# Performance work log

Measured on AMD Instinct MI355X. Metric: run time of the kernel, lower is better.

Reference implementation:

```python
import jax, jax.numpy as jnp
import numpy as np

B, L, D = 8, 4096, 768
EPS = 1e-5


def layer_norm(x, g, b):
    mu = jnp.mean(x, axis=-1, keepdims=True)
    var = jnp.mean(jnp.square(x - mu), axis=-1, keepdims=True)
    return (x - mu) * jax.lax.rsqrt(var + EPS) * g + b


def conv1d_same(x_blc, w_oik, b_o):
    # x_blc: [B, L, C] -> torch Conv1d(C, C, 3, padding=1) on [B, C, L]
    x_ncw = jnp.swapaxes(x_blc, 1, 2)
    y = jax.lax.conv_general_dilated(
        x_ncw, w_oik, window_strides=(1,), padding=[(1, 1)],
        dimension_numbers=("NCW", "OIW", "NCW"))
    y = y + b_o[None, :, None]
    return jnp.swapaxes(y, 1, 2)


def simple_ssm(u, a_p, b_p, c_p, d_p):
    # Diagonal SSM: h_t = sigmoid(a)*h_{t-1} + b*u_t ; y_t = c*h_t + d*u_t
    a = jax.nn.sigmoid(a_p)  # [D]

    def step(h, ut):  # h, ut: [B, D]
        h = a * h + b_p * ut
        return h, c_p * h

    h0 = jnp.zeros((u.shape[0], u.shape[2]), u.dtype)
    _, y = jax.lax.scan(step, h0, jnp.swapaxes(u, 0, 1))  # y: [L, B, D]
    return jnp.swapaxes(y, 0, 1) + d_p * u


def setup_inputs() -> dict:
    key = jax.random.key(0)
    ks = jax.random.split(key, 16)
    s_lin = 1.0 / np.sqrt(D)
    s_conv = 1.0 / np.sqrt(3 * D)
    return {
        "x": jax.random.normal(ks[0], (B, L, D), jnp.float32),
        "ln_g": jnp.ones((D,), jnp.float32),
        "ln_b": jnp.zeros((D,), jnp.float32),
        "Wi": jax.random.normal(ks[1], (D, 2 * D), jnp.float32) * s_lin,
        "bi": jnp.zeros((2 * D,), jnp.float32),
        "Wf_conv": jax.random.normal(ks[2], (D, D, 3), jnp.float32) * s_conv,
        "bf_conv": jnp.zeros((D,), jnp.float32),
        "af": jax.random.normal(ks[3], (D,), jnp.float32),
        "bf": jax.random.normal(ks[4], (D,), jnp.float32) * 0.5,
        "cf": jax.random.normal(ks[5], (D,), jnp.float32) * 0.5,
        "df": jax.random.normal(ks[6], (D,), jnp.float32) * 0.5,
        "Wb_conv": jax.random.normal(ks[7], (D, D, 3), jnp.float32) * s_conv,
        "bb_conv": jnp.zeros((D,), jnp.float32),
        "ab": jax.random.normal(ks[8], (D,), jnp.float32),
        "bb": jax.random.normal(ks[9], (D,), jnp.float32) * 0.5,
        "cb": jax.random.normal(ks[10], (D,), jnp.float32) * 0.5,
        "db": jax.random.normal(ks[11], (D,), jnp.float32) * 0.5,
        "Wo": jax.random.normal(ks[12], (D, D), jnp.float32) * s_lin,
        "bo": jnp.zeros((D,), jnp.float32),
    }


def reference(x, ln_g, ln_b, Wi, bi, Wf_conv, bf_conv, af, bf, cf, df,
              Wb_conv, bb_conv, ab, bb, cb, db, Wo, bo):
    residual = x
    xn = layer_norm(x, ln_g, ln_b)
    proj = xn @ Wi + bi                      # [B, L, 2D]
    xg, z = proj[..., :D], proj[..., D:]
    # forward branch
    f = conv1d_same(xg, Wf_conv, bf_conv)
    f = simple_ssm(f, af, bf, cf, df)
    # backward branch (flip along sequence)
    b_in = jnp.flip(xg, axis=1)
    bb_out = conv1d_same(b_in, Wb_conv, bb_conv)
    bb_out = simple_ssm(bb_out, ab, bb, cb, db)
    bb_out = jnp.flip(bb_out, axis=1)
    zg = jax.nn.silu(z)
    y = f * zg + bb_out * zg
    return y @ Wo + bo + residual
```

## Files before the change

kernel.cpp:

```cpp
#include <hip/hip_runtime.h>
#include <cstdint>
#include <cstddef>
#include <math.h>

#define L_SEQ 4096
#define D_DIM 768
#define B_SZ 8
#define M_ROWS (B_SZ * L_SEQ)
#define CHUNK 64

typedef __bf16 bf16x8 __attribute__((ext_vector_type(8)));
typedef float floatx4 __attribute__((ext_vector_type(4)));

#define GLP(p)  ((__attribute__((address_space(1))) const void*)(const void*)(p))
#define LDSP(p) ((__attribute__((address_space(3))) void*)(void*)(p))

__global__ __launch_bounds__(256) void ln_kernel(const float* __restrict__ x,
                                                 const float* __restrict__ g,
                                                 const float* __restrict__ b,
                                                 __bf16* __restrict__ xn) {
  __shared__ float red[256];
  const int tid = threadIdx.x;
  const size_t row = blockIdx.x;
  const float* xr = x + row * D_DIM;
  float v0 = xr[tid];
  float v1 = xr[tid + 256];
  float v2 = xr[tid + 512];
  red[tid] = v0 + v1 + v2;
  __syncthreads();
  for (int off = 128; off > 0; off >>= 1) {
    if (tid < off) red[tid] += red[tid + off];
    __syncthreads();
  }
  float mu = red[0] * (1.0f / D_DIM);
  __syncthreads();
  float d0 = v0 - mu, d1 = v1 - mu, d2 = v2 - mu;
  red[tid] = d0 * d0 + d1 * d1 + d2 * d2;
  __syncthreads();
  for (int off = 128; off > 0; off >>= 1) {
    if (tid < off) red[tid] += red[tid + off];
    __syncthreads();
  }
  float rs = rsqrtf(red[0] * (1.0f / D_DIM) + 1e-5f);
  __bf16* xo = xn + row * D_DIM;
  xo[tid]       = (__bf16)(d0 * rs * g[tid]       + b[tid]);
  xo[tid + 256] = (__bf16)(d1 * rs * g[tid + 256] + b[tid + 256]);
  xo[tid + 512] = (__bf16)(d2 * rs * g[tid + 512] + b[tid + 512]);
}


#define VMW(n) asm volatile("s_waitcnt vmcnt(" #n ")" ::: "memory")
#define BARR   asm volatile("s_barrier" ::: "memory")
#define MF(a, b, c) __builtin_amdgcn_mfma_f32_16x16x32_bf16((a), (b), (c), 0, 0, 0)
#define LDV(off) (*(const bf16x8*)(smem + (off)))

#define RDA(BUF, MOFF) do { \
  aR0k0 = LDV((BUF)*65536 + aoff + (MOFF) + ck0);        aR0k1 = LDV((BUF)*65536 + aoff + (MOFF) + ck1); \
  aR1k0 = LDV((BUF)*65536 + aoff + (MOFF) + 2048 + ck0); aR1k1 = LDV((BUF)*65536 + aoff + (MOFF) + 2048 + ck1); \
  aR2k0 = LDV((BUF)*65536 + aoff + (MOFF) + 4096 + ck0); aR2k1 = LDV((BUF)*65536 + aoff + (MOFF) + 4096 + ck1); \
  aR3k0 = LDV((BUF)*65536 + aoff + (MOFF) + 6144 + ck0); aR3k1 = LDV((BUF)*65536 + aoff + (MOFF) + 6144 + ck1); \
} while (0)

#define RDB01(BUF) do { \
  bN0k0 = LDV((BUF)*65536 + boff + ck0);        bN0k1 = LDV((BUF)*65536 + boff + ck1); \
  bN1k0 = LDV((BUF)*65536 + boff + 2048 + ck0); bN1k1 = LDV((BUF)*65536 + boff + 2048 + ck1); \
} while (0)

#define RDB23(BUF) do { \
  bN2k0 = LDV((BUF)*65536 + boff + 4096 + ck0); bN2k1 = LDV((BUF)*65536 + boff + 4096 + ck1); \
  bN3k0 = LDV((BUF)*65536 + boff + 6144 + ck0); bN3k1 = LDV((BUF)*65536 + boff + 6144 + ck1); \
} while (0)

#define MMQ01(AI) do { \
  acc[(AI)+0][0] = MF(aR0k0, bN0k0, acc[(AI)+0][0]); acc[(AI)+0][0] = MF(aR0k1, bN0k1, acc[(AI)+0][0]); \
  acc[(AI)+0][1] = MF(aR0k0, bN1k0, acc[(AI)+0][1]); acc[(AI)+0][1] = MF(aR0k1, bN1k1, acc[(AI)+0][1]); \
  acc[(AI)+1][0] = MF(aR1k0, bN0k0, acc[(AI)+1][0]); acc[(AI)+1][0] = MF(aR1k1, bN0k1, acc[(AI)+1][0]); \
  acc[(AI)+1][1] = MF(aR1k0, bN1k0, acc[(AI)+1][1]); acc[(AI)+1][1] = MF(aR1k1, bN1k1, acc[(AI)+1][1]); \
  acc[(AI)+2][0] = MF(aR2k0, bN0k0, acc[(AI)+2][0]); acc[(AI)+2][0] = MF(aR2k1, bN0k1, acc[(AI)+2][0]); \
  acc[(AI)+2][1] = MF(aR2k0, bN1k0, acc[(AI)+2][1]); acc[(AI)+2][1] = MF(aR2k1, bN1k1, acc[(AI)+2][1]); \
  acc[(AI)+3][0] = MF(aR3k0, bN0k0, acc[(AI)+3][0]); acc[(AI)+3][0] = MF(aR3k1, bN0k1, acc[(AI)+3][0]); \
  acc[(AI)+3][1] = MF(aR3k0, bN1k0, acc[(AI)+3][1]); acc[(AI)+3][1] = MF(aR3k1, bN1k1, acc[(AI)+3][1]); \
} while (0)

#define MMQ23(AI) do { \
  acc[(AI)+0][2] = MF(aR0k0, bN2k0, acc[(AI)+0][2]); acc[(AI)+0][2] = MF(aR0k1, bN2k1, acc[(AI)+0][2]); \
  acc[(AI)+0][3] = MF(aR0k0, bN3k0, acc[(AI)+0][3]); acc[(AI)+0][3] = MF(aR0k1, bN3k1, acc[(AI)+0][3]); \
  acc[(AI)+1][2] = MF(aR1k0, bN2k0, acc[(AI)+1][2]); acc[(AI)+1][2] = MF(aR1k1, bN2k1, acc[(AI)+1][2]); \
  acc[(AI)+1][3] = MF(aR1k0, bN3k0, acc[(AI)+1][3]); acc[(AI)+1][3] = MF(aR1k1, bN3k1, acc[(AI)+1][3]); \
  acc[(AI)+2][2] = MF(aR2k0, bN2k0, acc[(AI)+2][2]); acc[(AI)+2][2] = MF(aR2k1, bN2k1, acc[(AI)+2][2]); \
  acc[(AI)+2][3] = MF(aR2k0, bN3k0, acc[(AI)+2][3]); acc[(AI)+2][3] = MF(aR2k1, bN3k1, acc[(AI)+2][3]); \
  acc[(AI)+3][2] = MF(aR3k0, bN2k0, acc[(AI)+3][2]); acc[(AI)+3][2] = MF(aR3k1, bN2k1, acc[(AI)+3][2]); \
  acc[(AI)+3][3] = MF(aR3k0, bN3k0, acc[(AI)+3][3]); acc[(AI)+3][3] = MF(aR3k1, bN3k1, acc[(AI)+3][3]); \
} while (0)

#define STAGE_A_HP(h, p, tkt, BUF) do { \
  const __bf16* _s; \
  if (MODE == 1) { \
    const int _kb = ((tkt) * 43) >> 9;                        \
    const int _io = (((tkt) - _kb * 12) << 6) + (_kb - 1) * D_DIM; \
    _s = ((unsigned)(lv##h##p + _kb - 1) < (unsigned)L_SEQ) ? (rb##h##p + _io) : zbuf; \
  } else { \
    _s = rb##h##p + (tkt) * 64; \
  } \
  __builtin_amdgcn_global_load_lds(GLP(_s), \
      LDSP(smem + (BUF)*65536 + (h)*8192 + (p)*16384 + dstw), 16, 0, 0); \
} while (0)

#define STAGE_B_HP(h, p, tkt, BUF) \
  __builtin_amdgcn_global_load_lds(GLP(pB##h##p + (tkt) * 64), \
      LDSP(smem + (BUF)*65536 + 32768 + (h)*16384 + (p)*8192 + dstw), 16, 0, 0)

#define TILE(T, BUF, VA, VC, SA1, SREST) do { \
   \
  VMW(VA); BARR; \
  RDB01(BUF); RDA(BUF, 0); \
  if (SA1) { STAGE_A_HP(1, 0, (T) + 1, (BUF) ^ 1); STAGE_A_HP(1, 1, (T) + 1, (BUF) ^ 1); } \
  __builtin_amdgcn_s_setprio(1); MMQ01(0); __builtin_amdgcn_s_setprio(0); \
   \
  BARR; \
  RDB23(BUF); \
  if (SREST) { STAGE_A_HP(0, 0, (T) + 2, (BUF)); STAGE_A_HP(0, 1, (T) + 2, (BUF)); } \
  __builtin_amdgcn_s_setprio(1); MMQ23(0); __builtin_amdgcn_s_setprio(0); \
   \
  VMW(VC); BARR; \
  RDA(BUF, 8192); \
  if (SREST) { STAGE_B_HP(0, 0, (T) + 2, (BUF)); STAGE_B_HP(0, 1, (T) + 2, (BUF)); } \
  __builtin_amdgcn_s_setprio(1); MMQ01(4); __builtin_amdgcn_s_setprio(0); \
   \
  if (SREST) { STAGE_B_HP(1, 0, (T) + 2, (BUF)); STAGE_B_HP(1, 1, (T) + 2, (BUF)); } \
  __builtin_amdgcn_s_setprio(1); MMQ23(4); __builtin_amdgcn_s_setprio(0); \
} while (0)

template<int MODE, int NT, int NN>
__global__ __launch_bounds__(512) void gemm256_kernel(
    const __bf16* __restrict__ A, const __bf16* __restrict__ Bt,
    const float* __restrict__ bias_lo, const float* __restrict__ bias_hi,
    const float* __restrict__ resid,
    __bf16* __restrict__ out0, __bf16* __restrict__ out1,
    float* __restrict__ outf, const __bf16* __restrict__ zbuf) {
  extern __shared__ char smem[];
  constexpr int K = NT * 64;
  constexpr int nwg = NN * (M_ROWS / 256);
  constexpr int cpx = nwg / 8;
  const int bid = blockIdx.x;
  const int wgs = (bid & 7) * cpx + (bid >> 3);
  const int tileN = wgs % NN;
  const int tileM = wgs / NN;
  const int tid  = (int)threadIdx.x;
  const int w    = tid >> 6;
  const int lane = tid & 63;
  const int l15  = lane & 15;
  const int quad = lane >> 4;
  const int wm   = w >> 2;
  const int wn   = w & 3;

  const int srow = tid >> 3;
  const int ce   = ((tid & 7) ^ (srow & 7)) << 3;
  const int dstw = w << 10;

  const int aoff = (wm * 128 + l15) * 128;
  const int boff = 32768 + (wn * 64 + l15) * 128;
  const int ck0  = (quad ^ (l15 & 7)) << 4;
  const int ck1  = ((4 | quad) ^ (l15 & 7)) << 4;

  const __bf16* pB00 = Bt + (size_t)(tileN * 256 + srow) * K + ce;
  const __bf16* pB01 = Bt + (size_t)(tileN * 256 + 64 + srow) * K + ce;
  const __bf16* pB10 = Bt + (size_t)(tileN * 256 + 128 + srow) * K + ce;
  const __bf16* pB11 = Bt + (size_t)(tileN * 256 + 192 + srow) * K + ce;

  const __bf16 *rb00, *rb01, *rb10, *rb11;
  int lv00 = 0, lv01 = 0, lv10 = 0, lv11 = 0;
  {
    const int g00 = tileM * 256 + srow;
    const int g01 = tileM * 256 + 128 + srow;
    const int g10 = tileM * 256 + 64 + srow;
    const int g11 = tileM * 256 + 192 + srow;
    if (MODE == 1) {
      rb00 = A + (size_t)g00 * D_DIM + ce; lv00 = g00 & (L_SEQ - 1);
      rb01 = A + (size_t)g01 * D_DIM + ce; lv01 = g01 & (L_SEQ - 1);
      rb10 = A + (size_t)g10 * D_DIM + ce; lv10 = g10 & (L_SEQ - 1);
      rb11 = A + (size_t)g11 * D_DIM + ce; lv11 = g11 & (L_SEQ - 1);
    } else {
      rb00 = A + (size_t)g00 * K + ce;
      rb01 = A + (size_t)g01 * K + ce;
      rb10 = A + (size_t)g10 * K + ce;
      rb11 = A + (size_t)g11 * K + ce;
    }
  }

  bf16x8 aR0k0, aR0k1, aR1k0, aR1k1, aR2k0, aR2k1, aR3k0, aR3k1;
  bf16x8 bN0k0, bN0k1, bN1k0, bN1k1, bN2k0, bN2k1, bN3k0, bN3k1;
  floatx4 acc[8][4];
#pragma unroll
  for (int i = 0; i < 8; ++i)
#pragma unroll
    for (int j = 0; j < 4; ++j)
#pragma unroll
      for (int r = 0; r < 4; ++r) acc[i][j][r] = 0.0f;

  STAGE_A_HP(0, 0, 0, 0); STAGE_A_HP(0, 1, 0, 0);
  STAGE_B_HP(0, 0, 0, 0); STAGE_B_HP(0, 1, 0, 0);
  STAGE_B_HP(1, 0, 0, 0); STAGE_B_HP(1, 1, 0, 0);
  STAGE_A_HP(1, 0, 0, 0); STAGE_A_HP(1, 1, 0, 0);
  STAGE_A_HP(0, 0, 1, 1); STAGE_A_HP(0, 1, 1, 1);
  STAGE_B_HP(0, 0, 1, 1); STAGE_B_HP(0, 1, 1, 1);
  STAGE_B_HP(1, 0, 1, 1); STAGE_B_HP(1, 1, 1, 1);

  for (int it = 0; it < (NT - 2) / 2; ++it) {
    const int T0 = it * 2;
    TILE(T0,     0, 8, 10, 1, 1);
    TILE(T0 + 1, 1, 8, 10, 1, 1);
  }
  TILE(NT - 2, 0, 8, 8, 1, 0);
  TILE(NT - 1, 1, 2, 0, 0, 0);

  const int rowb = tileM * 256 + wm * 128 + quad * 4;
  const int colb = tileN * 256 + wn * 64 + l15;
#pragma unroll
  for (int mi = 0; mi < 8; ++mi) {
#pragma unroll
    for (int nj = 0; nj < 4; ++nj) {
      const int col = colb + nj * 16;
      float bv;
      if (MODE == 3) bv = bias_lo[col];
      else bv = (col < D_DIM) ? bias_lo[col] : bias_hi[col - D_DIM];
#pragma unroll
      for (int r = 0; r < 4; ++r) {
        const int row = rowb + mi * 16 + r;
        float v = acc[mi][nj][r] + bv;
        if (MODE == 3) {
          const size_t o = (size_t)row * D_DIM + col;
          outf[o] = v + resid[o];
        } else if (MODE == 0) {
          if (col < D_DIM) out0[(size_t)row * D_DIM + col] = (__bf16)v;
          else out1[(size_t)row * D_DIM + (col - D_DIM)] = (__bf16)(v / (1.0f + expf(-v)));
        } else {
          if (col < D_DIM) out0[(size_t)row * D_DIM + col] = (__bf16)v;
          else out1[(size_t)row * D_DIM + (col - D_DIM)] = (__bf16)v;
        }
      }
    }
  }
}

__global__ __launch_bounds__(256) void scan1_kernel(
    const float* __restrict__ ap0, const float* __restrict__ bp0,
    const float* __restrict__ ap1, const float* __restrict__ bp1,
    const __bf16* __restrict__ u0, const __bf16* __restrict__ u1,
    float* __restrict__ hl) {
  int idx = blockIdx.x * 256 + threadIdx.x;
  int dg = idx % 96;
  int rest = idx / 96;
  int chunk = rest & 63;
  int tb = rest >> 6;
  int tensor = tb >> 3;
  int b = tb & 7;
  const float* ap = (tensor ? ap1 : ap0) + dg * 8;
  const float* bp = (tensor ? bp1 : bp0) + dg * 8;
  const __bf16* u = (tensor ? u1 : u0) +
      ((size_t)(b * L_SEQ + chunk * CHUNK + (tensor ? CHUNK - 1 : 0))) * D_DIM + dg * 8;
  const int st = tensor ? -D_DIM : D_DIM;
  float a[8], bb[8], h[8];
#pragma unroll
  for (int j = 0; j < 8; ++j) {
    a[j] = 1.0f / (1.0f + expf(-ap[j]));
    bb[j] = bp[j];
    h[j] = 0.0f;
  }
  for (int t = 0; t < CHUNK; ++t) {
    bf16x8 uv = *(const bf16x8*)u;
#pragma unroll
    for (int j = 0; j < 8; ++j) h[j] = a[j] * h[j] + bb[j] * (float)uv[j];
    u += st;
  }
  float* o = hl + (size_t)(tb * 64 + chunk) * D_DIM + dg * 8;
#pragma unroll
  for (int j = 0; j < 8; ++j) o[j] = h[j];
}

__global__ __launch_bounds__(256) void scan2_kernel(
    const float* __restrict__ ap0, const float* __restrict__ ap1,
    float* __restrict__ hl) {
  int idx = blockIdx.x * 256 + threadIdx.x;
  int d = idx % D_DIM;
  int tb = idx / D_DIM;
  int tensor = tb >> 3;
  const float* ap = tensor ? ap1 : ap0;
  float a = 1.0f / (1.0f + expf(-ap[d]));
  float aT = a * a;  aT *= aT;  aT *= aT;  aT *= aT;  aT *= aT;  aT *= aT;
  float* p = hl + (size_t)tb * 64 * D_DIM + d + (tensor ? 63 * D_DIM : 0);
  const int st = tensor ? -D_DIM : D_DIM;
  float carry = 0.0f;
  for (int c = 0; c < 64; ++c) {
    float tmp = *p;
    *p = carry;
    carry = aT * carry + tmp;
    p += st;
  }
}

__global__ __launch_bounds__(256) void scan3_kernel(
    const float* __restrict__ ap0, const float* __restrict__ bp0,
    const float* __restrict__ cp0, const float* __restrict__ dp0,
    const float* __restrict__ ap1, const float* __restrict__ bp1,
    const float* __restrict__ cp1, const float* __restrict__ dp1,
    __bf16* __restrict__ u0, __bf16* __restrict__ u1,
    const float* __restrict__ hl) {
  int idx = blockIdx.x * 256 + threadIdx.x;
  int dg = idx % 96;
  int rest = idx / 96;
  int chunk = rest & 63;
  int tb = rest >> 6;
  int tensor = tb >> 3;
  int b = tb & 7;
  const float* ap = (tensor ? ap1 : ap0) + dg * 8;
  const float* bp = (tensor ? bp1 : bp0) + dg * 8;
  const float* cp = (tensor ? cp1 : cp0) + dg * 8;
  const float* dp = (tensor ? dp1 : dp0) + dg * 8;
  __bf16* u = (tensor ? u1 : u0) +
      ((size_t)(b * L_SEQ + chunk * CHUNK + (tensor ? CHUNK - 1 : 0))) * D_DIM + dg * 8;
  const int st = tensor ? -D_DIM : D_DIM;
  const float* hp = hl + (size_t)(tb * 64 + chunk) * D_DIM + dg * 8;
  float a[8], bb[8], cc[8], dd[8], h[8];
#pragma unroll
  for (int j = 0; j < 8; ++j) {
    a[j] = 1.0f / (1.0f + expf(-ap[j]));
    bb[j] = bp[j]; cc[j] = cp[j]; dd[j] = dp[j];
    h[j] = hp[j];
  }
  for (int t = 0; t < CHUNK; ++t) {
    bf16x8 uv = *(const bf16x8*)u;
    bf16x8 ov;
#pragma unroll
    for (int j = 0; j < 8; ++j) {
      float xv = (float)uv[j];
      h[j] = a[j] * h[j] + bb[j] * xv;
      ov[j] = (__bf16)(cc[j] * h[j] + dd[j] * xv);
    }
    *(bf16x8*)u = ov;
    u += st;
  }
}

__global__ __launch_bounds__(256) void gate_kernel(const __bf16* __restrict__ f,
                                                   const __bf16* __restrict__ bbuf,
                                                   const __bf16* __restrict__ zg,
                                                   __bf16* __restrict__ y) {
  size_t e = ((size_t)blockIdx.x * 256 + threadIdx.x) * 8;
  bf16x8 f8 = *(const bf16x8*)(f + e);
  bf16x8 b8 = *(const bf16x8*)(bbuf + e);
  bf16x8 z8 = *(const bf16x8*)(zg + e);
  bf16x8 o;
#pragma unroll
  for (int j = 0; j < 8; ++j)
    o[j] = (__bf16)(((float)f8[j] + (float)b8[j]) * (float)z8[j]);
  *(bf16x8*)(y + e) = o;
}

__global__ __launch_bounds__(256) void tr_kernel(const float* __restrict__ in,
                                                 __bf16* __restrict__ out,
                                                 int Kdim, int Ndim) {
  int idx = blockIdx.x * 256 + threadIdx.x;
  if (idx >= Kdim * Ndim) return;
  int n = idx / Kdim;
  int k = idx - n * Kdim;
  out[idx] = (__bf16)in[(size_t)k * Ndim + n];
}

__global__ __launch_bounds__(256) void trconv_kernel(const float* __restrict__ in,
                                                     __bf16* __restrict__ out,
                                                     int rev) {
  int idx = blockIdx.x * 256 + threadIdx.x;
  if (idx >= D_DIM * 2304) return;
  int o = idx / 2304;
  int rem = idx - o * 2304;
  int k = rem / D_DIM;
  int i = rem - k * D_DIM;
  int ks = rev ? (2 - k) : k;
  out[idx] = (__bf16)in[(size_t)o * 2304 + i * 3 + ks];
}

__global__ void zero_kernel(__bf16* z) { z[threadIdx.x] = (__bf16)0.0f; }

extern "C" void kernel_launch(void* const* d_in, const int* in_sizes, int n_in,
                              void* d_out, int out_size, void* d_ws, size_t ws_size,
                              hipStream_t stream) {
  const float* x    = (const float*)d_in[0];
  const float* ln_g = (const float*)d_in[1];
  const float* ln_b = (const float*)d_in[2];
  const float* Wi   = (const float*)d_in[3];
  const float* bi   = (const float*)d_in[4];
  const float* Wf   = (const float*)d_in[5];
  const float* bfc  = (const float*)d_in[6];
  const float* af   = (const float*)d_in[7];
  const float* bfp  = (const float*)d_in[8];
  const float* cfp  = (const float*)d_in[9];
  const float* dfp  = (const float*)d_in[10];
  const float* Wb   = (const float*)d_in[11];
  const float* bbc  = (const float*)d_in[12];
  const float* ab   = (const float*)d_in[13];
  const float* bbp  = (const float*)d_in[14];
  const float* cbp  = (const float*)d_in[15];
  const float* dbp  = (const float*)d_in[16];
  const float* Wo   = (const float*)d_in[17];
  const float* bo   = (const float*)d_in[18];
  float* out = (float*)d_out;

  char* ws = (char*)d_ws;
  const size_t BLD = (size_t)B_SZ * L_SEQ * D_DIM;
  __bf16* ws0 = (__bf16*)(ws);
  __bf16* ws1 = (__bf16*)(ws + BLD * 2);
  __bf16* ws2 = (__bf16*)(ws + BLD * 4);
  __bf16* ws3 = (__bf16*)(ws + BLD * 6);
  __bf16* wit  = (__bf16*)(ws + BLD * 8);
  __bf16* wcat = wit + (size_t)1536 * 768;
  __bf16* wot  = wcat + (size_t)1536 * 2304;
  __bf16* zbuf = wot + (size_t)768 * 768;
  float* hl = (float*)(ws + BLD * 2);
  const size_t needed = BLD * 8 +
      ((size_t)1536 * 768 + (size_t)1536 * 2304 + (size_t)768 * 768) * 2 + 256;
  if (ws_size < needed) return;

  static bool attr_done = false;
  if (!attr_done) {
    (void)hipFuncSetAttribute(reinterpret_cast<const void*>(&gemm256_kernel<0, 12, 6>),
                              hipFuncAttributeMaxDynamicSharedMemorySize, 131072);
    (void)hipFuncSetAttribute(reinterpret_cast<const void*>(&gemm256_kernel<1, 36, 6>),
                              hipFuncAttributeMaxDynamicSharedMemorySize, 131072);
    (void)hipFuncSetAttribute(reinterpret_cast<const void*>(&gemm256_kernel<3, 12, 3>),
                              hipFuncAttributeMaxDynamicSharedMemorySize, 131072);
    attr_done = true;
  }

  zero_kernel<<<1, 128, 0, stream>>>(zbuf);
  tr_kernel<<<(768 * 1536 + 255) / 256, 256, 0, stream>>>(Wi, wit, 768, 1536);
  trconv_kernel<<<(768 * 2304 + 255) / 256, 256, 0, stream>>>(Wf, wcat, 0);
  trconv_kernel<<<(768 * 2304 + 255) / 256, 256, 0, stream>>>(Wb, wcat + (size_t)768 * 2304, 1);
  tr_kernel<<<(768 * 768 + 255) / 256, 256, 0, stream>>>(Wo, wot, 768, 768);

  ln_kernel<<<M_ROWS, 256, 0, stream>>>(x, ln_g, ln_b, ws0);

  gemm256_kernel<0, 12, 6><<<768, 512, 131072, stream>>>(
      ws0, wit, bi, bi + 768, nullptr, ws1, ws2, nullptr, zbuf);

  gemm256_kernel<1, 36, 6><<<768, 512, 131072, stream>>>(
      ws1, wcat, bfc, bbc, nullptr, ws0, ws3, nullptr, zbuf);

  scan1_kernel<<<384, 256, 0, stream>>>(af, bfp, ab, bbp, ws0, ws3, hl);
  scan2_kernel<<<48, 256, 0, stream>>>(af, ab, hl);
  scan3_kernel<<<384, 256, 0, stream>>>(af, bfp, cfp, dfp, ab, bbp, cbp, dbp, ws0, ws3, hl);

  gate_kernel<<<12288, 256, 0, stream>>>(ws0, ws3, ws2, ws1);

  gemm256_kernel<3, 12, 3><<<384, 512, 131072, stream>>>(
      ws1, wot, bo, bo, x, nullptr, nullptr, out, zbuf);
}
```

Before: 746.4 us.

## Fuse SSM output pass with gating into one kernel

The final SSM scan pass and the elementwise gate kernel are merged. Each thread first runs the forward-branch scan in place, then runs the backward-branch scan and combines it directly with the forward result and the SiLU gate, writing the gated output. This drops the backward-branch output write and the separate gate kernel's reads, and removes one launch. To make room, the chunk-carry buffer moves into the now-unused conv weight area, since the gate output buffer it used to share is written during the same kernel. In exchange the grid is halved to 192 blocks, each thread doing two sequential 64-step chains, which lowers parallelism and latency hiding.

New measurement: 773.5 us. +3.6%, slower.

```diff
diff --git a/kernel.cpp b/kernel.cpp
--- a/kernel.cpp
+++ b/kernel.cpp
@@ -299,62 +299,83 @@
   }
 }
 
-__global__ __launch_bounds__(256) void scan3_kernel(
+__global__ __launch_bounds__(256) void ssm_gate_kernel(
     const float* __restrict__ ap0, const float* __restrict__ bp0,
     const float* __restrict__ cp0, const float* __restrict__ dp0,
     const float* __restrict__ ap1, const float* __restrict__ bp1,
     const float* __restrict__ cp1, const float* __restrict__ dp1,
-    __bf16* __restrict__ u0, __bf16* __restrict__ u1,
+    __bf16* __restrict__ u0, const __bf16* __restrict__ u1,
+    const __bf16* __restrict__ zg, __bf16* __restrict__ y,
     const float* __restrict__ hl) {
   int idx = blockIdx.x * 256 + threadIdx.x;
   int dg = idx % 96;
   int rest = idx / 96;
   int chunk = rest & 63;
-  int tb = rest >> 6;
-  int tensor = tb >> 3;
-  int b = tb & 7;
-  const float* ap = (tensor ? ap1 : ap0) + dg * 8;
-  const float* bp = (tensor ? bp1 : bp0) + dg * 8;
-  const float* cp = (tensor ? cp1 : cp0) + dg * 8;
-  const float* dp = (tensor ? dp1 : dp0) + dg * 8;
-  __bf16* u = (tensor ? u1 : u0) +
-      ((size_t)(b * L_SEQ + chunk * CHUNK + (tensor ? CHUNK - 1 : 0))) * D_DIM + dg * 8;
-  const int st = tensor ? -D_DIM : D_DIM;
-  const float* hp = hl + (size_t)(tb * 64 + chunk) * D_DIM + dg * 8;
-  float a[8], bb[8], cc[8], dd[8], h[8];
-#pragma unroll
-  for (int j = 0; j < 8; ++j) {
-    a[j] = 1.0f / (1.0f + expf(-ap[j]));
-    bb[j] = bp[j]; cc[j] = cp[j]; dd[j] = dp[j];
-    h[j] = hp[j];
-  }
-  for (int t = 0; t < CHUNK; ++t) {
-    bf16x8 uv = *(const bf16x8*)u;
-    bf16x8 ov;
+  int b = rest >> 6;
+  const size_t rowbase = (size_t)(b * L_SEQ + chunk * CHUNK) * D_DIM + dg * 8;
+
+  {
+    const float* ap = ap0 + dg * 8;
+    const float* bp = bp0 + dg * 8;
+    const float* cp = cp0 + dg * 8;
+    const float* dp = dp0 + dg * 8;
+    const float* hp = hl + (size_t)(b * 64 + chunk) * D_DIM + dg * 8;
+    float a[8], bb[8], cc[8], dd[8], h[8];
 #pragma unroll
     for (int j = 0; j < 8; ++j) {
-      float xv = (float)uv[j];
-      h[j] = a[j] * h[j] + bb[j] * xv;
-      ov[j] = (__bf16)(cc[j] * h[j] + dd[j] * xv);
-    }
-    *(bf16x8*)u = ov;
-    u += st;
-  }
-}
-
-__global__ __launch_bounds__(256) void gate_kernel(const __bf16* __restrict__ f,
-                                                   const __bf16* __restrict__ bbuf,
-                                                   const __bf16* __restrict__ zg,
-                                                   __bf16* __restrict__ y) {
-  size_t e = ((size_t)blockIdx.x * 256 + threadIdx.x) * 8;
-  bf16x8 f8 = *(const bf16x8*)(f + e);
-  bf16x8 b8 = *(const bf16x8*)(bbuf + e);
-  bf16x8 z8 = *(const bf16x8*)(zg + e);
-  bf16x8 o;
-#pragma unroll
-  for (int j = 0; j < 8; ++j)
-    o[j] = (__bf16)(((float)f8[j] + (float)b8[j]) * (float)z8[j]);
-  *(bf16x8*)(y + e) = o;
+      a[j] = 1.0f / (1.0f + expf(-ap[j]));
+      bb[j] = bp[j]; cc[j] = cp[j]; dd[j] = dp[j];
+      h[j] = hp[j];
+    }
+    __bf16* p = u0 + rowbase;
+    for (int t = 0; t < CHUNK; ++t) {
+      bf16x8 uv = *(const bf16x8*)p;
+      bf16x8 ov;
+#pragma unroll
+      for (int j = 0; j < 8; ++j) {
+        float xv = (float)uv[j];
+        h[j] = a[j] * h[j] + bb[j] * xv;
+        ov[j] = (__bf16)(cc[j] * h[j] + dd[j] * xv);
+      }
+      *(bf16x8*)p = ov;
+      p += D_DIM;
+    }
+  }
+
+  {
+    const float* ap = ap1 + dg * 8;
+    const float* bp = bp1 + dg * 8;
+    const float* cp = cp1 + dg * 8;
+    const float* dp = dp1 + dg * 8;
+    const float* hp = hl + (size_t)((8 + b) * 64 + chunk) * D_DIM + dg * 8;
+    float a[8], bb[8], cc[8], dd[8], h[8];
+#pragma unroll
+    for (int j = 0; j < 8; ++j) {
+      a[j] = 1.0f / (1.0f + expf(-ap[j]));
+      bb[j] = bp[j]; cc[j] = cp[j]; dd[j] = dp[j];
+      h[j] = hp[j];
+    }
+    const size_t tail = rowbase + (size_t)(CHUNK - 1) * D_DIM;
+    const __bf16* p1 = u1 + tail;
+    const __bf16* pf = u0 + tail;
+    const __bf16* pz = zg + tail;
+    __bf16* py = y + tail;
+    for (int t = 0; t < CHUNK; ++t) {
+      bf16x8 uv = *(const bf16x8*)p1;
+      bf16x8 f8 = *(const bf16x8*)pf;
+      bf16x8 z8 = *(const bf16x8*)pz;
+      bf16x8 ov;
+#pragma unroll
+      for (int j = 0; j < 8; ++j) {
+        float xv = (float)uv[j];
+        h[j] = a[j] * h[j] + bb[j] * xv;
+        float bbv = cc[j] * h[j] + dd[j] * xv;
+        ov[j] = (__bf16)(((float)f8[j] + bbv) * (float)z8[j]);
+      }
+      *(bf16x8*)py = ov;
+      p1 -= D_DIM; pf -= D_DIM; pz -= D_DIM; py -= D_DIM;
+    }
+  }
 }
 
 __global__ __launch_bounds__(256) void tr_kernel(const float* __restrict__ in,
@@ -416,7 +437,7 @@
   __bf16* wcat = wit + (size_t)1536 * 768;
   __bf16* wot  = wcat + (size_t)1536 * 2304;
   __bf16* zbuf = wot + (size_t)768 * 768;
-  float* hl = (float*)(ws + BLD * 2);
+  float* hl = (float*)wcat;
   const size_t needed = BLD * 8 +
       ((size_t)1536 * 768 + (size_t)1536 * 2304 + (size_t)768 * 768) * 2 + 256;
   if (ws_size < needed) return;
@@ -448,9 +469,8 @@
 
   scan1_kernel<<<384, 256, 0, stream>>>(af, bfp, ab, bbp, ws0, ws3, hl);
   scan2_kernel<<<48, 256, 0, stream>>>(af, ab, hl);
-  scan3_kernel<<<384, 256, 0, stream>>>(af, bfp, cfp, dfp, ab, bbp, cbp, dbp, ws0, ws3, hl);
-
-  gate_kernel<<<12288, 256, 0, stream>>>(ws0, ws3, ws2, ws1);
+  ssm_gate_kernel<<<192, 256, 0, stream>>>(af, bfp, cfp, dfp, ab, bbp, cbp, dbp,
+                                           ws0, ws3, ws2, ws1, hl);
 
   gemm256_kernel<3, 12, 3><<<384, 512, 131072, stream>>>(
       ws1, wot, bo, bo, x, nullptr, nullptr, out, zbuf);
```
